# Kernel optimization log

Hardware: AMD Instinct MI355X
Metric: run time of the kernel (lower is better)

Reference implementation:

```python
import jax, jax.numpy as jnp
import numpy as np

B, S, D = 4, 2048, 512
H, DK = 8, 64
FFN = 2048
LEFT, CHUNK, RIGHT = 512, 128, 128
EPS = 1e-5


def _emformer_mask():
    # True = disallowed. Each query attends to its own chunk, LEFT keys before
    # the chunk start, and RIGHT keys after the chunk end.
    idx = jnp.arange(S)
    cs = (idx // CHUNK) * CHUNK                      # chunk start per query
    j = idx[None, :]
    allowed = (j >= cs[:, None] - LEFT) & (j < cs[:, None] + CHUNK + RIGHT)
    return jnp.broadcast_to(~allowed, (B, 1, S, S))


def _ln(x, g, b):
    m = jnp.mean(x, axis=-1, keepdims=True)
    v = jnp.var(x, axis=-1, keepdims=True)
    return (x - m) * jax.lax.rsqrt(v + EPS) * g + b


def setup_inputs() -> dict:
    key = jax.random.key(0)
    ks = jax.random.split(key, 8)
    w = lambda k, shp: jax.random.normal(k, shp, dtype=jnp.float32) * 0.02
    return {
        "x": jax.random.normal(ks[0], (B, S, D), dtype=jnp.float32),
        "mask": _emformer_mask(),
        "ln_in_g": jnp.ones((D,), jnp.float32), "ln_in_b": jnp.zeros((D,), jnp.float32),
        "wq": w(ks[1], (D, D)), "bq": jnp.zeros((D,), jnp.float32),
        "wk": w(ks[2], (D, D)), "bk": jnp.zeros((D,), jnp.float32),
        "wv": w(ks[3], (D, D)), "bv": jnp.zeros((D,), jnp.float32),
        "ln1_g": jnp.ones((D,), jnp.float32), "ln1_b": jnp.zeros((D,), jnp.float32),
        "w1": w(ks[4], (D, FFN)), "b1": jnp.zeros((FFN,), jnp.float32),
        "w2": w(ks[5], (FFN, D)), "b2": jnp.zeros((D,), jnp.float32),
        "ln2_g": jnp.ones((D,), jnp.float32), "ln2_b": jnp.zeros((D,), jnp.float32),
    }


def reference(x, mask, ln_in_g, ln_in_b, wq, bq, wk, bk, wv, bv,
              ln1_g, ln1_b, w1, b1, w2, b2, ln2_g, ln2_b):
    h = _ln(x, ln_in_g, ln_in_b)                                  # [B,S,D]
    q = (h @ wq + bq).reshape(B, S, H, DK).transpose(0, 2, 1, 3)   # [B,H,S,DK]
    k = (h @ wk + bk).reshape(B, S, H, DK).transpose(0, 2, 1, 3)
    v = (h @ wv + bv).reshape(B, S, H, DK).transpose(0, 2, 1, 3)
    scores = jnp.einsum("bhqd,bhkd->bhqk", q, k) / np.sqrt(DK).astype(np.float32)
    scores = jnp.where(mask, -jnp.inf, scores)
    probs = jax.nn.softmax(scores, axis=-1)
    probs = jnp.where(mask, 0.0, probs)                           # masked_fill after softmax
    out = jnp.einsum("bhqk,bhkd->bhqd", probs, v)
    out = out.transpose(0, 2, 1, 3).reshape(B, S, D)
    attn_out = out + h                                            # residual uses post-LN input
    o = _ln(attn_out, ln1_g, ln1_b)
    o = (o @ w1 + b1) @ w2 + b2 + attn_out                        # NOTE: no activation in source
    return _ln(o, ln2_g, ln2_b)
```

## Files before the change

kernel.cpp:

```cpp
#include <hip/hip_runtime.h>
#include <stdint.h>

#define B_ 4
#define S_ 2048
#define D_ 512
#define H_ 8
#define FFN_ 2048
#define M_ (B_*S_)

typedef unsigned short u16;
typedef __attribute__((ext_vector_type(8))) __bf16 bf16x8;
typedef __attribute__((ext_vector_type(8))) u16 u16x8;
typedef __attribute__((ext_vector_type(4))) float f32x4;

__device__ __forceinline__ u16 f2bf(float f) {
  uint32_t u = __builtin_bit_cast(uint32_t, f);
  u += 0x7FFFu + ((u >> 16) & 1u);
  return (u16)(u >> 16);
}
__device__ __forceinline__ bf16x8 ldfrag(const u16* p) {
  return __builtin_bit_cast(bf16x8, *(const u16x8*)p);
}
__device__ __forceinline__ void gld16(const void* g, void* l) {
  __builtin_amdgcn_global_load_lds(
      (const __attribute__((address_space(1))) void*)g,
      (__attribute__((address_space(3))) void*)l, 16, 0, 0);
}

__global__ __launch_bounds__(256)
void wtrans(const float* __restrict__ W, int K, int N, u16* __restrict__ Wt) {
  __shared__ float t[32][33];
  int n0 = blockIdx.x * 32, k0 = blockIdx.y * 32;
  int x = threadIdx.x, y = threadIdx.y;
#pragma unroll
  for (int r = 0; r < 4; r++) t[y + 8*r][x] = W[(size_t)(k0 + y + 8*r) * N + n0 + x];
  __syncthreads();
#pragma unroll
  for (int r = 0; r < 4; r++) Wt[(size_t)(n0 + y + 8*r) * K + k0 + x] = f2bf(t[x][y + 8*r]);
}

__global__ void bcat(const float* __restrict__ bq, const float* __restrict__ bk,
                     const float* __restrict__ bv, float* __restrict__ o) {
  int i = blockIdx.x * 256 + threadIdx.x;
  o[i] = i < 512 ? bq[i] : (i < 1024 ? bk[i - 512] : bv[i - 1024]);
}

template <bool OUT32, bool OUT16>
__global__ __launch_bounds__(128)
void ln_k(const float* __restrict__ x, const float* __restrict__ g,
          const float* __restrict__ bta, float* __restrict__ y32, u16* __restrict__ y16) {
  int row = blockIdx.x;
  int t = threadIdx.x;
  const float* xr = x + (size_t)row * 512;
  f32x4 v = *(const f32x4*)(xr + t * 4);
  float s = v.x + v.y + v.z + v.w;
  float s2 = v.x*v.x + v.y*v.y + v.z*v.z + v.w*v.w;
#pragma unroll
  for (int m = 32; m; m >>= 1) { s += __shfl_xor(s, m); s2 += __shfl_xor(s2, m); }
  __shared__ float p[4];
  int wv = t >> 6;
  if ((t & 63) == 0) { p[wv] = s; p[2 + wv] = s2; }
  __syncthreads();
  s = p[0] + p[1]; s2 = p[2] + p[3];
  float mean = s * (1.f / 512.f);
  float var = s2 * (1.f / 512.f) - mean * mean;
  float rs = rsqrtf(var + 1e-5f);
#pragma unroll
  for (int j = 0; j < 4; j++) {
    float o = (v[j] - mean) * rs * g[t*4 + j] + bta[t*4 + j];
    if constexpr (OUT32) y32[(size_t)row * 512 + t*4 + j] = o;
    if constexpr (OUT16) y16[(size_t)row * 512 + t*4 + j] = f2bf(o);
  }
}

template <int NTW, int NCOL, bool RESID, bool OUT32, bool OUT16>
__global__ __launch_bounds__(256)
void gemm_bt(const u16* __restrict__ A, const u16* __restrict__ Bt,
             const float* __restrict__ bias, int K, int N,
             const float* __restrict__ resid, float* __restrict__ C32,
             u16* __restrict__ C16) {
  __shared__ __align__(16) u16 As[128 * 32];
  __shared__ __align__(16) u16 Bs[NTW * 1024];
  const int tid = threadIdx.x;
  const int wave = tid >> 6, lane = tid & 63;
  const int l15 = lane & 15, quad = lane >> 4;
  const int wm = wave >> 1, wn = wave & 1;

  const int lin = blockIdx.x;
  const int rpx = (M_ / 128) / 8;
  const int xcd = lin & 7, local = lin >> 3;
  const int row0 = (xcd * rpx + local / NCOL) * 128;
  const int col0 = (local % NCOL) * (NTW * 32);

  f32x4 acc[4][NTW];
#pragma unroll
  for (int i = 0; i < 4; i++)
#pragma unroll
    for (int j = 0; j < NTW; j++) acc[i][j] = (f32x4){0.f, 0.f, 0.f, 0.f};

  const int lr = lane >> 2;
  const int lc = ((lane & 3) ^ ((lane >> 3) & 3)) * 8;
  const u16* aG0 = A + (size_t)(row0 + (wave * 2) * 16 + lr) * K + lc;
  const u16* aG1 = A + (size_t)(row0 + (wave * 2 + 1) * 16 + lr) * K + lc;
  u16* aL0 = As + (wave * 2) * 512 + lane * 8;
  u16* aL1 = As + (wave * 2 + 1) * 512 + lane * 8;
  const u16* bG[NTW / 2];
  u16* bL[NTW / 2];
#pragma unroll
  for (int i = 0; i < NTW / 2; i++) {
    int ch = wave * (NTW / 2) + i;
    bG[i] = Bt + (size_t)(col0 + ch * 16 + lr) * K + lc;
    bL[i] = Bs + ch * 512 + lane * 8;
  }
  const int rsw = (l15 >> 1) & 3;

  for (int k0 = 0; k0 < K; k0 += 32) {
    __syncthreads();
    gld16(aG0 + k0, aL0);
    gld16(aG1 + k0, aL1);
#pragma unroll
    for (int i = 0; i < NTW / 2; i++) gld16(bG[i] + k0, bL[i]);
    __syncthreads();
    bf16x8 af[4], bf[NTW];
#pragma unroll
    for (int mt = 0; mt < 4; mt++)
      af[mt] = ldfrag(As + (wm * 64 + mt * 16 + l15) * 32 + ((quad ^ rsw) * 8));
#pragma unroll
    for (int nt = 0; nt < NTW; nt++)
      bf[nt] = ldfrag(Bs + (wn * (NTW * 16) + nt * 16 + l15) * 32 + ((quad ^ rsw) * 8));
#pragma unroll
    for (int mt = 0; mt < 4; mt++)
#pragma unroll
      for (int nt = 0; nt < NTW; nt++)
        acc[mt][nt] = __builtin_amdgcn_mfma_f32_16x16x32_bf16(af[mt], bf[nt], acc[mt][nt], 0, 0, 0);
  }
#pragma unroll
  for (int mt = 0; mt < 4; mt++)
#pragma unroll
    for (int nt = 0; nt < NTW; nt++) {
      int n = col0 + wn * (NTW * 16) + nt * 16 + l15;
      float bv = bias[n];
#pragma unroll
      for (int r = 0; r < 4; r++) {
        int m = row0 + wm * 64 + mt * 16 + quad * 4 + r;
        float val = acc[mt][nt][r] + bv;
        if constexpr (RESID) val += resid[(size_t)m * N + n];
        if constexpr (OUT32) C32[(size_t)m * N + n] = val;
        if constexpr (OUT16) C16[(size_t)m * N + n] = f2bf(val);
      }
    }
}

__global__ __launch_bounds__(256)
void vtrans(const u16* __restrict__ qkv, u16* __restrict__ vt) {
  __shared__ u16 t[64][65];
  int s0 = blockIdx.x * 64, h = blockIdx.y, b = blockIdx.z;
  int x = threadIdx.x, y = threadIdx.y;
  const u16* src = qkv + (size_t)(b * 2048 + s0) * 1536 + 1024 + h * 64;
#pragma unroll
  for (int r = 0; r < 16; r++) { int s = y + 4*r; t[s][x] = src[(size_t)s * 1536 + x]; }
  __syncthreads();
  u16* dst = vt + (size_t)((b * 8 + h) * 64) * 2048 + s0;
#pragma unroll
  for (int r = 0; r < 16; r++) { int d = y + 4*r; dst[(size_t)d * 2048 + x] = t[x][d]; }
}

#define PSTR 136
__global__ __launch_bounds__(256)
void attn_k(const u16* __restrict__ qkv, const u16* __restrict__ vt,
            const float* __restrict__ hres, float* __restrict__ attn) {
  __shared__ __align__(16) u16 smem[8192 + 8192 + 128 * PSTR];
  u16* Ks = smem;
  u16* Vts = smem + 8192;
  u16* Ps = smem + 16384;
  u16* Qs = Ps;

  const int c = blockIdx.x, hh = blockIdx.y, b = blockIdx.z;
  const int s0 = c * 128;
  const int tid = threadIdx.x, wave = tid >> 6, lane = tid & 63;
  const int l15 = lane & 15, quad = lane >> 4;
  const int t_lo = (c > 4) ? c - 4 : 0;
  const int t_hi = (c + 2 < 16) ? c + 2 : 16;
  const int l7sw = l15 & 7;

  {
    const int cg = ((lane & 7) ^ (lane >> 3)) * 8;
    const int cp = (lane & 7) * 8;
#pragma unroll
    for (int q2 = 0; q2 < 4; q2++) {
      int r = wave * 32 + q2 * 8 + (lane >> 3);
      gld16(qkv + (size_t)(b * 2048 + s0 + r) * 1536 + hh * 64 + cg, Qs + r * 64 + cp);
    }
  }
  __syncthreads();
  bf16x8 qf[2][2];
#pragma unroll
  for (int qg = 0; qg < 2; qg++)
#pragma unroll
    for (int f = 0; f < 2; f++)
      qf[qg][f] = ldfrag(Qs + (qg * 64 + wave * 16 + l15) * 64 + (((f * 4 + quad) ^ l7sw) * 8));

  f32x4 accO[2][4];
#pragma unroll
  for (int qg = 0; qg < 2; qg++)
#pragma unroll
    for (int i = 0; i < 4; i++) accO[qg][i] = (f32x4){0.f, 0.f, 0.f, 0.f};
  float den[2][4] = {{0.f, 0.f, 0.f, 0.f}, {0.f, 0.f, 0.f, 0.f}};

  for (int kt = t_lo; kt < t_hi; ++kt) {
    __syncthreads();
    {
      const int cgk = ((lane & 7) ^ (lane >> 3)) * 8;
      const int cpk = (lane & 7) * 8;
#pragma unroll
      for (int q2 = 0; q2 < 4; q2++) {
        int r = wave * 32 + q2 * 8 + (lane >> 3);
        gld16(qkv + (size_t)(b * 2048 + kt * 128 + r) * 1536 + 512 + hh * 64 + cgk,
              Ks + r * 64 + cpk);
      }
      const int cpv = (lane & 15) * 8;
#pragma unroll
      for (int q2 = 0; q2 < 4; q2++) {
        int d = (wave * 4 + q2) * 4 + (lane >> 4);
        int cgv = ((lane & 8) | ((lane & 7) ^ (lane >> 4) ^ ((q2 & 1) << 2))) * 8;
        gld16(vt + (size_t)((b * 8 + hh) * 64 + d) * 2048 + kt * 128 + cgv,
              Vts + d * 128 + cpv);
      }
    }
    __syncthreads();

#pragma unroll
    for (int nt = 0; nt < 8; nt++) {
      bf16x8 kf0 = ldfrag(Ks + (nt * 16 + l15) * 64 + ((quad ^ l7sw) * 8));
      bf16x8 kf1 = ldfrag(Ks + (nt * 16 + l15) * 64 + (((4 + quad) ^ l7sw) * 8));
#pragma unroll
      for (int qg = 0; qg < 2; qg++) {
        f32x4 s4 = (f32x4){0.f, 0.f, 0.f, 0.f};
        s4 = __builtin_amdgcn_mfma_f32_16x16x32_bf16(qf[qg][0], kf0, s4, 0, 0, 0);
        s4 = __builtin_amdgcn_mfma_f32_16x16x32_bf16(qf[qg][1], kf1, s4, 0, 0, 0);
#pragma unroll
        for (int r = 0; r < 4; r++) {
          float pp = exp2f(s4[r] * (1.4426950408889634f * 0.125f));
          den[qg][r] += pp;
          Ps[(qg * 64 + wave * 16 + quad * 4 + r) * PSTR + nt * 16 + l15] = f2bf(pp);
        }
      }
    }
#pragma unroll
    for (int ki = 0; ki < 4; ki++) {
      bf16x8 pf[2];
#pragma unroll
      for (int qg = 0; qg < 2; qg++)
        pf[qg] = ldfrag(Ps + (qg * 64 + wave * 16 + l15) * PSTR + (ki * 4 + quad) * 8);
#pragma unroll
      for (int dt = 0; dt < 4; dt++) {
        int g = ki * 4 + quad;
        bf16x8 vf = ldfrag(Vts + (dt * 16 + l15) * 128 + (((g & 8) | ((g & 7) ^ l7sw)) * 8));
#pragma unroll
        for (int qg = 0; qg < 2; qg++)
          accO[qg][dt] = __builtin_amdgcn_mfma_f32_16x16x32_bf16(pf[qg], vf, accO[qg][dt], 0, 0, 0);
      }
    }
  }
#pragma unroll
  for (int qg = 0; qg < 2; qg++)
#pragma unroll
    for (int r = 0; r < 4; r++) {
      float d = den[qg][r];
      d += __shfl_xor(d, 1); d += __shfl_xor(d, 2);
      d += __shfl_xor(d, 4); d += __shfl_xor(d, 8);
      den[qg][r] = d;
    }
#pragma unroll
  for (int qg = 0; qg < 2; qg++)
#pragma unroll
    for (int dt = 0; dt < 4; dt++)
#pragma unroll
      for (int r = 0; r < 4; r++) {
        int m = s0 + qg * 64 + wave * 16 + quad * 4 + r;
        size_t idx = (size_t)(b * 2048 + m) * 512 + hh * 64 + dt * 16 + l15;
        attn[idx] = accO[qg][dt][r] / den[qg][r] + hres[idx];
      }
}

extern "C" void kernel_launch(void* const* d_in, const int* in_sizes, int n_in,
                              void* d_out, int out_size, void* d_ws, size_t ws_size,
                              hipStream_t stream) {
  (void)in_sizes; (void)n_in; (void)out_size; (void)ws_size;
  const float* x       = (const float*)d_in[0];
  const float* ln_in_g = (const float*)d_in[2];
  const float* ln_in_b = (const float*)d_in[3];
  const float* wq = (const float*)d_in[4];
  const float* bq = (const float*)d_in[5];
  const float* wk = (const float*)d_in[6];
  const float* bk = (const float*)d_in[7];
  const float* wv = (const float*)d_in[8];
  const float* bv = (const float*)d_in[9];
  const float* ln1_g = (const float*)d_in[10];
  const float* ln1_b = (const float*)d_in[11];
  const float* w1 = (const float*)d_in[12];
  const float* b1 = (const float*)d_in[13];
  const float* w2 = (const float*)d_in[14];
  const float* b2 = (const float*)d_in[15];
  const float* ln2_g = (const float*)d_in[16];
  const float* ln2_b = (const float*)d_in[17];

  char* ws = (char*)d_ws;
  size_t off = 0;
  auto alloc = [&](size_t bytes) {
    void* p = ws + off;
    off = (off + bytes + 255) & ~(size_t)255;
    return p;
  };
  u16*   wqkvt = (u16*)  alloc((size_t)1536 * 512 * 2);
  float* bqkv  = (float*)alloc(1536 * 4);
  u16*   w1t   = (u16*)  alloc((size_t)2048 * 512 * 2);
  u16*   w2t   = (u16*)  alloc((size_t)512 * 2048 * 2);
  float* h32   = (float*)alloc((size_t)M_ * 512 * 4);
  u16*   h16   = (u16*)  alloc((size_t)M_ * 512 * 2);
  u16*   qkv16 = (u16*)  alloc((size_t)M_ * 1536 * 2);
  u16*   vtb   = (u16*)  alloc((size_t)B_ * H_ * 64 * 2048 * 2);
  float* attn32= (float*)alloc((size_t)M_ * 512 * 4);
  float* out2  = h32;
  u16*   o16   = h16;
  u16*   f16b  = qkv16;

  wtrans<<<dim3(16, 16), dim3(32, 8), 0, stream>>>(wq, 512, 512, wqkvt);
  wtrans<<<dim3(16, 16), dim3(32, 8), 0, stream>>>(wk, 512, 512, wqkvt + (size_t)512 * 512);
  wtrans<<<dim3(16, 16), dim3(32, 8), 0, stream>>>(wv, 512, 512, wqkvt + (size_t)1024 * 512);
  wtrans<<<dim3(64, 16), dim3(32, 8), 0, stream>>>(w1, 512, 2048, w1t);
  wtrans<<<dim3(16, 64), dim3(32, 8), 0, stream>>>(w2, 2048, 512, w2t);
  bcat<<<6, 256, 0, stream>>>(bq, bk, bv, bqkv);

  ln_k<true, true><<<M_, 128, 0, stream>>>(x, ln_in_g, ln_in_b, h32, h16);
  gemm_bt<4, 12, false, false, true><<<dim3(12 * 64), 256, 0, stream>>>(
      h16, wqkvt, bqkv, 512, 1536, nullptr, nullptr, qkv16);
  vtrans<<<dim3(32, 8, 4), dim3(64, 4), 0, stream>>>(qkv16, vtb);
  attn_k<<<dim3(16, 8, 4), 256, 0, stream>>>(qkv16, vtb, h32, attn32);
  ln_k<false, true><<<M_, 128, 0, stream>>>(attn32, ln1_g, ln1_b, nullptr, o16);
  gemm_bt<4, 16, false, false, true><<<dim3(16 * 64), 256, 0, stream>>>(
      o16, w1t, b1, 512, 2048, nullptr, nullptr, f16b);
  gemm_bt<2, 8, true, true, false><<<dim3(8 * 64), 256, 0, stream>>>(
      f16b, w2t, b2, 2048, 512, attn32, out2, nullptr);
  ln_k<true, false><<<M_, 128, 0, stream>>>(out2, ln2_g, ln2_b, (float*)d_out, nullptr);
}
```

Measured before the change: 301.3 us.

## Replace LDS-staged GEMM with direct global-to-register loads and double buffering

```diff
diff --git a/kernel.cpp b/kernel.cpp
--- a/kernel.cpp
+++ b/kernel.cpp
@@ -75,12 +75,10 @@
 
 template <int NTW, int NCOL, bool RESID, bool OUT32, bool OUT16>
 __global__ __launch_bounds__(256)
-void gemm_bt(const u16* __restrict__ A, const u16* __restrict__ Bt,
+void gemm_rf(const u16* __restrict__ A, const u16* __restrict__ Bt,
              const float* __restrict__ bias, int K, int N,
              const float* __restrict__ resid, float* __restrict__ C32,
              u16* __restrict__ C16) {
-  __shared__ __align__(16) u16 As[128 * 32];
-  __shared__ __align__(16) u16 Bs[NTW * 1024];
   const int tid = threadIdx.x;
   const int wave = tid >> 6, lane = tid & 63;
   const int l15 = lane & 15, quad = lane >> 4;
@@ -92,48 +90,62 @@
   const int row0 = (xcd * rpx + local / NCOL) * 128;
   const int col0 = (local % NCOL) * (NTW * 32);
 
+  const u16* aP[4];
+#pragma unroll
+  for (int mt = 0; mt < 4; mt++)
+    aP[mt] = A + (size_t)(row0 + wm * 64 + mt * 16 + l15) * K + quad * 8;
+  const u16* bP[NTW];
+#pragma unroll
+  for (int nt = 0; nt < NTW; nt++)
+    bP[nt] = Bt + (size_t)(col0 + wn * (NTW * 16) + nt * 16 + l15) * K + quad * 8;
+
   f32x4 acc[4][NTW];
 #pragma unroll
   for (int i = 0; i < 4; i++)
 #pragma unroll
     for (int j = 0; j < NTW; j++) acc[i][j] = (f32x4){0.f, 0.f, 0.f, 0.f};
 
-  const int lr = lane >> 2;
-  const int lc = ((lane & 3) ^ ((lane >> 3) & 3)) * 8;
-  const u16* aG0 = A + (size_t)(row0 + (wave * 2) * 16 + lr) * K + lc;
-  const u16* aG1 = A + (size_t)(row0 + (wave * 2 + 1) * 16 + lr) * K + lc;
-  u16* aL0 = As + (wave * 2) * 512 + lane * 8;
-  u16* aL1 = As + (wave * 2 + 1) * 512 + lane * 8;
-  const u16* bG[NTW / 2];
-  u16* bL[NTW / 2];
-#pragma unroll
-  for (int i = 0; i < NTW / 2; i++) {
-    int ch = wave * (NTW / 2) + i;
-    bG[i] = Bt + (size_t)(col0 + ch * 16 + lr) * K + lc;
-    bL[i] = Bs + ch * 512 + lane * 8;
+  bf16x8 a0[4], b0[NTW], a1[4], b1[NTW];
+#pragma unroll
+  for (int mt = 0; mt < 4; mt++) a0[mt] = ldfrag(aP[mt]);
+#pragma unroll
+  for (int nt = 0; nt < NTW; nt++) b0[nt] = ldfrag(bP[nt]);
+
+  for (int k0 = 0; k0 + 64 < K; k0 += 64) {
+#pragma unroll
+    for (int mt = 0; mt < 4; mt++) a1[mt] = ldfrag(aP[mt] + k0 + 32);
+#pragma unroll
+    for (int nt = 0; nt < NTW; nt++) b1[nt] = ldfrag(bP[nt] + k0 + 32);
+#pragma unroll
+    for (int mt = 0; mt < 4; mt++)
+#pragma unroll
+      for (int nt = 0; nt < NTW; nt++)
+        acc[mt][nt] = __builtin_amdgcn_mfma_f32_16x16x32_bf16(a0[mt], b0[nt], acc[mt][nt], 0, 0, 0);
+#pragma unroll
+    for (int mt = 0; mt < 4; mt++) a0[mt] = ldfrag(aP[mt] + k0 + 64);
+#pragma unroll
+    for (int nt = 0; nt < NTW; nt++) b0[nt] = ldfrag(bP[nt] + k0 + 64);
+#pragma unroll
+    for (int mt = 0; mt < 4; mt++)
+#pragma unroll
+      for (int nt = 0; nt < NTW; nt++)
+        acc[mt][nt] = __builtin_amdgcn_mfma_f32_16x16x32_bf16(a1[mt], b1[nt], acc[mt][nt], 0, 0, 0);
   }
-  const int rsw = (l15 >> 1) & 3;
-
-  for (int k0 = 0; k0 < K; k0 += 32) {
-    __syncthreads();
-    gld16(aG0 + k0, aL0);
-    gld16(aG1 + k0, aL1);
-#pragma unroll
-    for (int i = 0; i < NTW / 2; i++) gld16(bG[i] + k0, bL[i]);
-    __syncthreads();
-    bf16x8 af[4], bf[NTW];
-#pragma unroll
-    for (int mt = 0; mt < 4; mt++)
-      af[mt] = ldfrag(As + (wm * 64 + mt * 16 + l15) * 32 + ((quad ^ rsw) * 8));
+#pragma unroll
+  for (int mt = 0; mt < 4; mt++) a1[mt] = ldfrag(aP[mt] + K - 32);
+#pragma unroll
+  for (int nt = 0; nt < NTW; nt++) b1[nt] = ldfrag(bP[nt] + K - 32);
+#pragma unroll
+  for (int mt = 0; mt < 4; mt++)
 #pragma unroll
     for (int nt = 0; nt < NTW; nt++)
-      bf[nt] = ldfrag(Bs + (wn * (NTW * 16) + nt * 16 + l15) * 32 + ((quad ^ rsw) * 8));
-#pragma unroll
-    for (int mt = 0; mt < 4; mt++)
-#pragma unroll
-      for (int nt = 0; nt < NTW; nt++)
-        acc[mt][nt] = __builtin_amdgcn_mfma_f32_16x16x32_bf16(af[mt], bf[nt], acc[mt][nt], 0, 0, 0);
-  }
+      acc[mt][nt] = __builtin_amdgcn_mfma_f32_16x16x32_bf16(a0[mt], b0[nt], acc[mt][nt], 0, 0, 0);
+#pragma unroll
+  for (int mt = 0; mt < 4; mt++)
+#pragma unroll
+    for (int nt = 0; nt < NTW; nt++)
+      acc[mt][nt] = __builtin_amdgcn_mfma_f32_16x16x32_bf16(a1[mt], b1[nt], acc[mt][nt], 0, 0, 0);
+
 #pragma unroll
   for (int mt = 0; mt < 4; mt++)
 #pragma unroll
@@ -333,14 +345,14 @@
   bcat<<<6, 256, 0, stream>>>(bq, bk, bv, bqkv);
 
   ln_k<true, true><<<M_, 128, 0, stream>>>(x, ln_in_g, ln_in_b, h32, h16);
-  gemm_bt<4, 12, false, false, true><<<dim3(12 * 64), 256, 0, stream>>>(
+  gemm_rf<4, 12, false, false, true><<<dim3(12 * 64), 256, 0, stream>>>(
       h16, wqkvt, bqkv, 512, 1536, nullptr, nullptr, qkv16);
   vtrans<<<dim3(32, 8, 4), dim3(64, 4), 0, stream>>>(qkv16, vtb);
   attn_k<<<dim3(16, 8, 4), 256, 0, stream>>>(qkv16, vtb, h32, attn32);
   ln_k<false, true><<<M_, 128, 0, stream>>>(attn32, ln1_g, ln1_b, nullptr, o16);
-  gemm_bt<4, 16, false, false, true><<<dim3(16 * 64), 256, 0, stream>>>(
+  gemm_rf<4, 16, false, false, true><<<dim3(16 * 64), 256, 0, stream>>>(
       o16, w1t, b1, 512, 2048, nullptr, nullptr, f16b);
-  gemm_bt<2, 8, true, true, false><<<dim3(8 * 64), 256, 0, stream>>>(
+  gemm_rf<2, 8, true, true, false><<<dim3(8 * 64), 256, 0, stream>>>(
       f16b, w2t, b2, 2048, 512, attn32, out2, nullptr);
   ln_k<true, false><<<M_, 128, 0, stream>>>(out2, ln2_g, ln2_b, (float*)d_out, nullptr);
 }
```

Result: slower. 410.2 us (+36.1%).
